# Kernel tuning notes

Hardware: AMD Instinct MI355X
Metric: run time of the kernel (lower is better)

The kernel has to match this reference:

```python
import jax, jax.numpy as jnp
import numpy as np

B, N, IN_F, H, DEG, L = 4096, 64, 32, 128, 8, 2
E = N * DEG
ALPHA = 0.2  # LeakyReLU slope
EPS = 1e-5   # LayerNorm eps


def setup_inputs() -> dict:
    key = jax.random.key(0)
    ks = jax.random.split(key, 16)
    # ring graph: node i -> (i+k) mod N for k=1..DEG (unique edges, every node has out-edges)
    src = jnp.repeat(jnp.arange(N, dtype=jnp.int32), DEG)
    dst = ((src + jnp.tile(jnp.arange(1, DEG + 1, dtype=jnp.int32), N)) % N).astype(jnp.int32)
    edge_index = jnp.stack([src, dst])  # (2, E)
    Hh = H // 2
    inp = {
        "x": jax.random.normal(ks[0], (B, IN_F), jnp.float32),
        "station_idx": jax.random.randint(ks[1], (B,), 0, N, jnp.int32),
        "edge_index": edge_index,
        "edge_weight": jax.random.uniform(ks[2], (E,), jnp.float32, 0.1, 1.0),
        "Wp": jax.random.normal(ks[3], (IN_F, H), jnp.float32) / np.sqrt(IN_F),
        "bp": jnp.zeros((H,), jnp.float32),
        "emb": jax.random.normal(ks[4], (N, Hh), jnp.float32) * 0.02,
        "gat_W": jax.random.normal(ks[5], (L, H, H), jnp.float32) / np.sqrt(H),
        "gat_a": jax.random.normal(ks[6], (L, 2 * H), jnp.float32) * 0.1,
        "W1": jax.random.normal(ks[7], (H + Hh, H), jnp.float32) / np.sqrt(H + Hh),
        "b1": jnp.zeros((H,), jnp.float32),
        "g1": jnp.ones((H,), jnp.float32),
        "be1": jnp.zeros((H,), jnp.float32),
        "W2": jax.random.normal(ks[8], (H, Hh), jnp.float32) / np.sqrt(H),
        "b2": jnp.zeros((Hh,), jnp.float32),
        "g2": jnp.ones((Hh,), jnp.float32),
        "be2": jnp.zeros((Hh,), jnp.float32),
        "Wo": jax.random.normal(ks[9], (Hh, 1), jnp.float32) / np.sqrt(Hh),
        "bo": jnp.zeros((1,), jnp.float32),
    }
    return inp


def _layernorm(v, g, b):
    m = v.mean(-1, keepdims=True)
    var = ((v - m) ** 2).mean(-1, keepdims=True)
    return (v - m) / jnp.sqrt(var + EPS) * g + b


def _gat(h, W, a, src, dst, edge_weight):
    # h: (B, N, H); W: (H, H); a: (2H,)
    Wh = jnp.einsum('bnf,fg->bng', h, W)
    s_src = Wh @ a[:H]   # (B, N)
    s_dst = Wh @ a[H:]   # (B, N)
    e = jax.nn.leaky_relu(s_src[:, src] + s_dst[:, dst], ALPHA)  # (B, E)
    e = e * edge_weight[None, :]
    att = jnp.zeros((h.shape[0], N, N), h.dtype).at[:, src, dst].set(e)
    mask = att == 0  # faithfully reproduces the torch zero-mask trick
    att = jnp.where(mask, -jnp.inf, att)
    att = jax.nn.softmax(att, axis=2)
    att = jnp.where(mask, 0.0, att)
    # dropout is identity at inference
    return jax.nn.elu(jnp.einsum('bnm,bmf->bnf', att, Wh))


def reference(x, station_idx, edge_index, edge_weight, Wp, bp, emb, gat_W, gat_a,
              W1, b1, g1, be1, W2, b2, g2, be2, Wo, bo):
    src, dst = edge_index[0], edge_index[1]
    h0 = x @ Wp + bp                               # (B, H)
    h = jnp.broadcast_to(h0[:, None, :], (x.shape[0], N, H))
    for i in range(L):
        h = h + _gat(h, gat_W[i], gat_a[i], src, dst, edge_weight)
    h_node = h[jnp.arange(x.shape[0]), station_idx]  # (B, H)
    s = emb[station_idx]                              # (B, H//2)
    z = jnp.concatenate([h_node, s], axis=-1)
    z = jax.nn.relu(_layernorm(z @ W1 + b1, g1, be1))
    z = jax.nn.relu(_layernorm(z @ W2 + b2, g2, be2))
    return (z @ Wo + bo).squeeze(-1)                  # (B,)
```

## Files before the change

kernel.cpp:

```cpp
#include <hip/hip_runtime.h>
#include <math.h>

namespace {

constexpr int SPW  = 8;
constexpr int ACTW = 196;
constexpr float LNEPS = 1e-5f;

typedef __attribute__((ext_vector_type(8))) __bf16 bf16x8;
typedef __attribute__((ext_vector_type(4))) float  f32x4;

template<int V> struct ic { static constexpr int value = V; };

template<int N, int I = 0, class F>
__device__ __forceinline__ void sfor(F&& f) {
    if constexpr (I < N) { f(ic<I>{}); sfor<N, I + 1>(f); }
}

__device__ __forceinline__ float elu1(float v) {
    return v > 0.f ? v : (__expf(v) - 1.f);
}

__global__ __launch_bounds__(64) void pack_weights(
    const float* __restrict__ Wp, const float* __restrict__ gatW,
    const float* __restrict__ W1, const float* __restrict__ W2,
    __bf16* __restrict__ wsf)
{
    const int f = blockIdx.x;
    const int l = threadIdx.x;
    const float* src; int kt, nt, N;
    if (f < 8)        { src = Wp;            kt = 0;            nt = f;            N = 128; }
    else if (f < 40)  { int r = f - 8;  src = gatW;         kt = r >> 3; nt = r & 7; N = 128; }
    else if (f < 72)  { int r = f - 40; src = gatW + 16384; kt = r >> 3; nt = r & 7; N = 128; }
    else if (f < 120) { int r = f - 72; src = W1;           kt = r / 8;  nt = r % 8; N = 128; }
    else              { int r = f - 120; src = W2;          kt = r >> 2; nt = r & 3; N = 64;  }
    const int k0 = kt * 32 + (l >> 4) * 8;
    const int n  = nt * 16 + (l & 15);
    bf16x8 v;
    sfor<8>([&](auto E) {
        v[E.value] = (__bf16)src[(size_t)(k0 + E.value) * N + n];
    });
    *reinterpret_cast<bf16x8*>(wsf + ((size_t)f * 64 + l) * 8) = v;
}

__global__ __launch_bounds__(128) void mfma_fused(
    const float* __restrict__ x, const int* __restrict__ sid,
    const __bf16* __restrict__ wsf,
    const float* __restrict__ bp, const float* __restrict__ emb,
    const float* __restrict__ b1, const float* __restrict__ g1,
    const float* __restrict__ be1,
    const float* __restrict__ b2, const float* __restrict__ g2,
    const float* __restrict__ be2,
    const float* __restrict__ Wo, const float* __restrict__ bo,
    float* __restrict__ out)
{
    __shared__ __align__(16) __bf16 wlds[128 * 512];
    __shared__ __align__(16) float  actbuf[2][16 * ACTW];

    const int tid = threadIdx.x;
    const int l   = tid & 63;
    const int w   = tid >> 6;
    const int gq  = l >> 4;
    const int j   = l & 15;
    const int sbase = (blockIdx.x * 2 + w) * SPW;
    float* A = actbuf[w];

    const int s  = l >> 2, ch = l & 3;
    float4 xv0 = {0,0,0,0}, xv1 = xv0;
    int st = 0;
    if (s < SPW) {
        const float* xp = x + (size_t)(sbase + s) * 32 + ch * 8;
        xv0 = *reinterpret_cast<const float4*>(xp);
        xv1 = *reinterpret_cast<const float4*>(xp + 4);
        st  = sid[sbase + s];
    }
    bf16x8 wpf[8];
    sfor<8>([&](auto NT) {
        wpf[NT.value] = *reinterpret_cast<const bf16x8*>(
            wsf + ((size_t)NT.value * 64 + l) * 8);
    });
    float bpv[8];
    sfor<8>([&](auto NT) { bpv[NT.value] = bp[NT.value * 16 + j]; });

    {
        const float4* gW = reinterpret_cast<const float4*>(wsf)
                         + (size_t)(8 + w * 64) * 64 + l;
        float4* sW = reinterpret_cast<float4*>(wlds) + (size_t)(w * 64) * 64 + l;
#pragma unroll 8
        for (int i = 0; i < 64; ++i) sW[(size_t)i * 64] = gW[(size_t)i * 64];
    }

    {
        float* dst = A + s * ACTW + ch * 8;
        *reinterpret_cast<float4*>(dst)     = xv0;
        *reinterpret_cast<float4*>(dst + 4) = xv1;
        float4 e0 = {0,0,0,0}, e1 = e0, e2 = e0, e3 = e0;
        if (s < SPW) {
            const float* ep = emb + (size_t)st * 64 + ch * 16;
            e0 = *reinterpret_cast<const float4*>(ep);
            e1 = *reinterpret_cast<const float4*>(ep + 4);
            e2 = *reinterpret_cast<const float4*>(ep + 8);
            e3 = *reinterpret_cast<const float4*>(ep + 12);
        }
        float* ed = A + s * ACTW + 128 + ch * 16;
        *reinterpret_cast<float4*>(ed)      = e0;
        *reinterpret_cast<float4*>(ed + 4)  = e1;
        *reinterpret_cast<float4*>(ed + 8)  = e2;
        *reinterpret_cast<float4*>(ed + 12) = e3;
    }
    __syncthreads();

    auto akt = [&]<int KT>(ic<KT>) -> bf16x8 {
        const float* p = A + j * ACTW + KT * 32 + gq * 8;
        const float4 f0 = *reinterpret_cast<const float4*>(p);
        const float4 f1 = *reinterpret_cast<const float4*>(p + 4);
        bf16x8 a;
        a[0] = (__bf16)f0.x; a[1] = (__bf16)f0.y; a[2] = (__bf16)f0.z; a[3] = (__bf16)f0.w;
        a[4] = (__bf16)f1.x; a[5] = (__bf16)f1.y; a[6] = (__bf16)f1.z; a[7] = (__bf16)f1.w;
        return a;
    };

    auto gemm = [&]<int NKT, int NNT>(ic<NKT>, ic<NNT>, int fbase, f32x4 (&acc)[NNT]) {
        const __bf16* fb = wlds + (size_t)fbase * 512 + (size_t)l * 8;
        bf16x8 bq0[NNT], bq1[NNT];
        auto ldkt = [&](auto KT, bf16x8 (&bq)[NNT]) {
            sfor<NNT>([&](auto NT) {
                bq[NT.value] = *reinterpret_cast<const bf16x8*>(
                    fb + (size_t)(decltype(KT)::value * NNT + NT.value) * 512);
            });
        };
        auto mm = [&](bf16x8 a, bf16x8 (&bq)[NNT]) {
            sfor<NNT>([&](auto NT) {
                acc[NT.value] = __builtin_amdgcn_mfma_f32_16x16x32_bf16(
                    a, bq[NT.value], acc[NT.value], 0, 0, 0);
            });
        };
        ldkt(ic<0>{}, bq0);
        sfor<NKT>([&](auto KT) {
            constexpr int kt = decltype(KT)::value;
            if constexpr (kt + 1 < NKT) {
                if constexpr (((kt + 1) & 1) == 0) ldkt(ic<kt + 1>{}, bq0);
                else                               ldkt(ic<kt + 1>{}, bq1);
            }
            const bf16x8 a = akt(ic<kt>{});
            if constexpr ((kt & 1) == 0) mm(a, bq0); else mm(a, bq1);
        });
    };

    auto writeC = [&](f32x4 (&C)[8]) {
        sfor<8>([&](auto NT) { sfor<4>([&](auto R) {
            A[(4 * gq + R.value) * ACTW + NT.value * 16 + j] = C[NT.value][R.value];
        }); });
    };

    f32x4 hC[8];

    {
        f32x4 acc[8] = {};
        const bf16x8 a = akt(ic<0>{});
        sfor<8>([&](auto NT) {
            acc[NT.value] = __builtin_amdgcn_mfma_f32_16x16x32_bf16(
                a, wpf[NT.value], acc[NT.value], 0, 0, 0);
        });
        sfor<8>([&](auto NT) { sfor<4>([&](auto R) {
            hC[NT.value][R.value] = acc[NT.value][R.value] + bpv[NT.value];
        }); });
    }
    writeC(hC);

    {
        f32x4 acc[8] = {};
        gemm(ic<4>{}, ic<8>{}, 0, acc);
        sfor<8>([&](auto NT) { sfor<4>([&](auto R) {
            hC[NT.value][R.value] += elu1(acc[NT.value][R.value]);
        }); });
    }
    writeC(hC);

    {
        f32x4 acc[8] = {};
        gemm(ic<4>{}, ic<8>{}, 32, acc);
        sfor<8>([&](auto NT) { sfor<4>([&](auto R) {
            hC[NT.value][R.value] += elu1(acc[NT.value][R.value]);
        }); });
    }
    writeC(hC);

    {
        f32x4 acc[8] = {};
        gemm(ic<6>{}, ic<8>{}, 64, acc);
        float b1v[8], g1v[8], be1v[8];
        sfor<8>([&](auto NT) {
            b1v[NT.value]  = b1[NT.value * 16 + j];
            g1v[NT.value]  = g1[NT.value * 16 + j];
            be1v[NT.value] = be1[NT.value * 16 + j];
        });
        float su[4] = {}, sq[4] = {};
        sfor<8>([&](auto NT) { sfor<4>([&](auto R) {
            const float u = acc[NT.value][R.value] + b1v[NT.value];
            acc[NT.value][R.value] = u;
            su[R.value] += u; sq[R.value] += u * u;
        }); });
#pragma unroll
        for (int off = 1; off <= 8; off <<= 1) {
            sfor<4>([&](auto R) {
                su[R.value] += __shfl_xor(su[R.value], off, 64);
                sq[R.value] += __shfl_xor(sq[R.value], off, 64);
            });
        }
        float m[4], rs[4];
        sfor<4>([&](auto R) {
            m[R.value] = su[R.value] * (1.f / 128.f);
            const float var = sq[R.value] * (1.f / 128.f) - m[R.value] * m[R.value];
            rs[R.value] = rsqrtf(var + LNEPS);
        });
        sfor<8>([&](auto NT) { sfor<4>([&](auto R) {
            const float z = fmaxf((acc[NT.value][R.value] - m[R.value]) * rs[R.value]
                                  * g1v[NT.value] + be1v[NT.value], 0.f);
            A[(4 * gq + R.value) * ACTW + NT.value * 16 + j] = z;
        }); });
    }

    {
        f32x4 acc[4] = {};
        gemm(ic<4>{}, ic<4>{}, 112, acc);
        float b2v[4], g2v[4], be2v[4], wov[4];
        sfor<4>([&](auto NT) {
            b2v[NT.value]  = b2[NT.value * 16 + j];
            g2v[NT.value]  = g2[NT.value * 16 + j];
            be2v[NT.value] = be2[NT.value * 16 + j];
            wov[NT.value]  = Wo[NT.value * 16 + j];
        });
        float su[4] = {}, sq[4] = {};
        sfor<4>([&](auto NT) { sfor<4>([&](auto R) {
            const float v = acc[NT.value][R.value] + b2v[NT.value];
            acc[NT.value][R.value] = v;
            su[R.value] += v; sq[R.value] += v * v;
        }); });
#pragma unroll
        for (int off = 1; off <= 8; off <<= 1) {
            sfor<4>([&](auto R) {
                su[R.value] += __shfl_xor(su[R.value], off, 64);
                sq[R.value] += __shfl_xor(sq[R.value], off, 64);
            });
        }
        float po[4];
        sfor<4>([&](auto R) {
            const float m   = su[R.value] * (1.f / 64.f);
            const float var = sq[R.value] * (1.f / 64.f) - m * m;
            const float rs  = rsqrtf(var + LNEPS);
            float p = 0.f;
            sfor<4>([&](auto NT) {
                p += fmaxf((acc[NT.value][R.value] - m) * rs * g2v[NT.value]
                           + be2v[NT.value], 0.f) * wov[NT.value];
            });
            po[R.value] = p;
        });
#pragma unroll
        for (int off = 1; off <= 8; off <<= 1) {
            sfor<4>([&](auto R) { po[R.value] += __shfl_xor(po[R.value], off, 64); });
        }
        const float bov = bo[0];
        if (j == 0 && gq < 2) {
            sfor<4>([&](auto R) {
                out[sbase + 4 * gq + R.value] = po[R.value] + bov;
            });
        }
    }
}

}

extern "C" void kernel_launch(void* const* d_in, const int* in_sizes, int n_in,
                              void* d_out, int out_size, void* d_ws, size_t ws_size,
                              hipStream_t stream)
{
    const float* x    = (const float*)d_in[0];
    const int*   sid  = (const int*)d_in[1];
    const float* Wp   = (const float*)d_in[4];
    const float* bp   = (const float*)d_in[5];
    const float* emb  = (const float*)d_in[6];
    const float* gatW = (const float*)d_in[7];
    const float* W1   = (const float*)d_in[9];
    const float* b1   = (const float*)d_in[10];
    const float* g1   = (const float*)d_in[11];
    const float* be1  = (const float*)d_in[12];
    const float* W2   = (const float*)d_in[13];
    const float* b2   = (const float*)d_in[14];
    const float* g2   = (const float*)d_in[15];
    const float* be2  = (const float*)d_in[16];
    const float* Wo   = (const float*)d_in[17];
    const float* bo   = (const float*)d_in[18];
    float* out = (float*)d_out;

    __bf16* wsf = (__bf16*)d_ws;

    pack_weights<<<dim3(136), dim3(64), 0, stream>>>(Wp, gatW, W1, W2, wsf);
    mfma_fused<<<dim3(4096 / (2 * SPW)), dim3(128), 0, stream>>>(
        x, sid, wsf, bp, emb, b1, g1, be1, b2, g2, be2, Wo, bo, out);
}
```

Baseline: 102.4 us.

## Read weights from global memory and shrink blocks to one wave of four samples

Removes the per-block staging of 128 KB of weight fragments into LDS. The B operands now come straight from global memory, where they should hit in L2. Each block becomes a single 64-thread wave handling 4 samples instead of two waves of 8 each, giving 1024 blocks and a small LDS footprint for higher occupancy. The GEMM K-loop and the GAT layers become runtime loops that are not unrolled, which cuts code size. The cost is that each MFMA tile now carries only 4 real rows out of 16, so more MFMA work is wasted, and the global weight loads add latency.

```diff
diff --git a/kernel.cpp b/kernel.cpp
--- a/kernel.cpp
+++ b/kernel.cpp
@@ -3,7 +3,7 @@
 
 namespace {
 
-constexpr int SPW  = 8;
+constexpr int SPW  = 4;
 constexpr int ACTW = 196;
 constexpr float LNEPS = 1e-5f;
 
@@ -43,7 +43,7 @@
     *reinterpret_cast<bf16x8*>(wsf + ((size_t)f * 64 + l) * 8) = v;
 }
 
-__global__ __launch_bounds__(128) void mfma_fused(
+__global__ __launch_bounds__(64) void mfma_fused(
     const float* __restrict__ x, const int* __restrict__ sid,
     const __bf16* __restrict__ wsf,
     const float* __restrict__ bp, const float* __restrict__ emb,
@@ -54,18 +54,14 @@
     const float* __restrict__ Wo, const float* __restrict__ bo,
     float* __restrict__ out)
 {
-    __shared__ __align__(16) __bf16 wlds[128 * 512];
-    __shared__ __align__(16) float  actbuf[2][16 * ACTW];
-
-    const int tid = threadIdx.x;
-    const int l   = tid & 63;
-    const int w   = tid >> 6;
-    const int gq  = l >> 4;
-    const int j   = l & 15;
-    const int sbase = (blockIdx.x * 2 + w) * SPW;
-    float* A = actbuf[w];
-
-    const int s  = l >> 2, ch = l & 3;
+    __shared__ __align__(16) float A[16 * ACTW];
+
+    const int l  = threadIdx.x;
+    const int gq = l >> 4;
+    const int j  = l & 15;
+    const int sbase = blockIdx.x * SPW;
+
+    const int s = l >> 2, ch = l & 3;
     float4 xv0 = {0,0,0,0}, xv1 = xv0;
     int st = 0;
     if (s < SPW) {
@@ -81,14 +77,6 @@
     });
     float bpv[8];
     sfor<8>([&](auto NT) { bpv[NT.value] = bp[NT.value * 16 + j]; });
-
-    {
-        const float4* gW = reinterpret_cast<const float4*>(wsf)
-                         + (size_t)(8 + w * 64) * 64 + l;
-        float4* sW = reinterpret_cast<float4*>(wlds) + (size_t)(w * 64) * 64 + l;
-#pragma unroll 8
-        for (int i = 0; i < 64; ++i) sW[(size_t)i * 64] = gW[(size_t)i * 64];
-    }
 
     {
         float* dst = A + s * ACTW + ch * 8;
@@ -108,10 +96,9 @@
         *reinterpret_cast<float4*>(ed + 8)  = e2;
         *reinterpret_cast<float4*>(ed + 12) = e3;
     }
-    __syncthreads();
-
-    auto akt = [&]<int KT>(ic<KT>) -> bf16x8 {
-        const float* p = A + j * ACTW + KT * 32 + gq * 8;
+
+    auto aktd = [&](int kt) -> bf16x8 {
+        const float* p = A + j * ACTW + kt * 32 + gq * 8;
         const float4 f0 = *reinterpret_cast<const float4*>(p);
         const float4 f1 = *reinterpret_cast<const float4*>(p + 4);
         bf16x8 a;
@@ -120,13 +107,14 @@
         return a;
     };
 
-    auto gemm = [&]<int NKT, int NNT>(ic<NKT>, ic<NNT>, int fbase, f32x4 (&acc)[NNT]) {
-        const __bf16* fb = wlds + (size_t)fbase * 512 + (size_t)l * 8;
+    auto gemm = [&]<int NNT>(ic<NNT>, int nkt, int fbase, f32x4 (&acc)[NNT]) {
+        asm volatile("" : "+s"(nkt));
+        const __bf16* fb = wsf + ((size_t)fbase * 64 + l) * 8;
         bf16x8 bq0[NNT], bq1[NNT];
-        auto ldkt = [&](auto KT, bf16x8 (&bq)[NNT]) {
+        auto ld = [&](int kt, bf16x8 (&bq)[NNT]) {
+            const __bf16* p = fb + (size_t)kt * (NNT * 512);
             sfor<NNT>([&](auto NT) {
-                bq[NT.value] = *reinterpret_cast<const bf16x8*>(
-                    fb + (size_t)(decltype(KT)::value * NNT + NT.value) * 512);
+                bq[NT.value] = *reinterpret_cast<const bf16x8*>(p + NT.value * 512);
             });
         };
         auto mm = [&](bf16x8 a, bf16x8 (&bq)[NNT]) {
@@ -135,16 +123,14 @@
                     a, bq[NT.value], acc[NT.value], 0, 0, 0);
             });
         };
-        ldkt(ic<0>{}, bq0);
-        sfor<NKT>([&](auto KT) {
-            constexpr int kt = decltype(KT)::value;
-            if constexpr (kt + 1 < NKT) {
-                if constexpr (((kt + 1) & 1) == 0) ldkt(ic<kt + 1>{}, bq0);
-                else                               ldkt(ic<kt + 1>{}, bq1);
-            }
-            const bf16x8 a = akt(ic<kt>{});
-            if constexpr ((kt & 1) == 0) mm(a, bq0); else mm(a, bq1);
-        });
+        ld(0, bq0);
+#pragma clang loop unroll(disable)
+        for (int kt = 0; kt < nkt; kt += 2) {
+            ld(kt + 1, bq1);
+            mm(aktd(kt), bq0);
+            if (kt + 2 < nkt) ld(kt + 2, bq0);
+            mm(aktd(kt + 1), bq1);
+        }
     };
 
     auto writeC = [&](f32x4 (&C)[8]) {
@@ -157,7 +143,7 @@
 
     {
         f32x4 acc[8] = {};
-        const bf16x8 a = akt(ic<0>{});
+        const bf16x8 a = aktd(0);
         sfor<8>([&](auto NT) {
             acc[NT.value] = __builtin_amdgcn_mfma_f32_16x16x32_bf16(
                 a, wpf[NT.value], acc[NT.value], 0, 0, 0);
@@ -169,26 +155,22 @@
     writeC(hC);
 
     {
+        int ngat = 2;
+        asm volatile("" : "+s"(ngat));
+#pragma clang loop unroll(disable)
+        for (int gi = 0; gi < ngat; ++gi) {
+            f32x4 acc[8] = {};
+            gemm(ic<8>{}, 4, 8 + gi * 32, acc);
+            sfor<8>([&](auto NT) { sfor<4>([&](auto R) {
+                hC[NT.value][R.value] += elu1(acc[NT.value][R.value]);
+            }); });
+            writeC(hC);
+        }
+    }
+
+    {
         f32x4 acc[8] = {};
-        gemm(ic<4>{}, ic<8>{}, 0, acc);
-        sfor<8>([&](auto NT) { sfor<4>([&](auto R) {
-            hC[NT.value][R.value] += elu1(acc[NT.value][R.value]);
-        }); });
-    }
-    writeC(hC);
-
-    {
-        f32x4 acc[8] = {};
-        gemm(ic<4>{}, ic<8>{}, 32, acc);
-        sfor<8>([&](auto NT) { sfor<4>([&](auto R) {
-            hC[NT.value][R.value] += elu1(acc[NT.value][R.value]);
-        }); });
-    }
-    writeC(hC);
-
-    {
-        f32x4 acc[8] = {};
-        gemm(ic<6>{}, ic<8>{}, 64, acc);
+        gemm(ic<8>{}, 6, 72, acc);
         float b1v[8], g1v[8], be1v[8];
         sfor<8>([&](auto NT) {
             b1v[NT.value]  = b1[NT.value * 16 + j];
@@ -223,7 +205,7 @@
 
     {
         f32x4 acc[4] = {};
-        gemm(ic<4>{}, ic<4>{}, 112, acc);
+        gemm(ic<4>{}, 4, 120, acc);
         float b2v[4], g2v[4], be2v[4], wov[4];
         sfor<4>([&](auto NT) {
             b2v[NT.value]  = b2[NT.value * 16 + j];
@@ -261,9 +243,9 @@
             sfor<4>([&](auto R) { po[R.value] += __shfl_xor(po[R.value], off, 64); });
         }
         const float bov = bo[0];
-        if (j == 0 && gq < 2) {
+        if (j == 0 && gq == 0) {
             sfor<4>([&](auto R) {
-                out[sbase + 4 * gq + R.value] = po[R.value] + bov;
+                out[sbase + R.value] = po[R.value] + bov;
             });
         }
     }
@@ -296,6 +278,6 @@
     __bf16* wsf = (__bf16*)d_ws;
 
     pack_weights<<<dim3(136), dim3(64), 0, stream>>>(Wp, gatW, W1, W2, wsf);
-    mfma_fused<<<dim3(4096 / (2 * SPW)), dim3(128), 0, stream>>>(
+    mfma_fused<<<dim3(4096 / SPW), dim3(64), 0, stream>>>(
         x, sid, wsf, bp, emb, b1, g1, be1, b2, g2, be2, Wo, bo, out);
 }
```

After: 101.2 us. No clear change (-1.2%).
